# Performance work log

Measured on AMD Instinct MI355X. Metric: run time of the kernel, lower is better.

## Reference

```python
import jax, jax.numpy as jnp
import numpy as np

B, N, C = 4, 2048, 1024
H = 16
D = C // H  # head_dim = 64
SCALE = 1.0 / np.sqrt(D).astype(np.float32)


def setup_inputs() -> dict:
    key = jax.random.key(0)
    ks = jax.random.split(key, 6)
    s = 0.02
    return {
        "x": jax.random.normal(ks[0], (B, N, C), dtype=jnp.float32),
        "Wq": jax.random.normal(ks[1], (C, C), dtype=jnp.float32) * s,
        "Wk": jax.random.normal(ks[2], (C, C), dtype=jnp.float32) * s,
        "Wv": jax.random.normal(ks[3], (C, C), dtype=jnp.float32) * s,
        "Wo": jax.random.normal(ks[4], (C, C), dtype=jnp.float32) * s,
        "bo": jax.random.normal(ks[5], (C,), dtype=jnp.float32) * s,
    }


def reference(x, Wq, Wk, Wv, Wo, bo):
    # q/k/v projections (no bias, qkv_bias=False), split heads -> [B,H,N,D]
    def heads(t):
        return t.reshape(B, N, H, D).transpose(0, 2, 1, 3)
    q = heads(x @ Wq)
    k = heads(x @ Wk)
    v = heads(x @ Wv)
    attn = jnp.einsum("bhnd,bhmd->bhnm", q, k) * SCALE  # [B,H,N,N]
    attn = jax.nn.softmax(attn, axis=-1)
    out = jnp.einsum("bhnm,bhmd->bhnd", attn, v)  # [B,H,N,D]
    out = out.transpose(0, 2, 1, 3).reshape(B, N, C)
    return out @ Wo + bo
```

## Files before the change

kernel.cpp:

```cpp
#include <hip/hip_runtime.h>
#include <hip/hip_bf16.h>


typedef __bf16 bf16x8 __attribute__((ext_vector_type(8)));
typedef __bf16 bf16x4 __attribute__((ext_vector_type(4)));
typedef float  f32x4  __attribute__((ext_vector_type(4)));
typedef float  f32x16 __attribute__((ext_vector_type(16)));
typedef unsigned int u32x4 __attribute__((ext_vector_type(4)));

#define LSCALE 0.18033688f
#define DEFER_THR 8.0f

__device__ __forceinline__ f32x4 mfma16(bf16x8 a, bf16x8 b, f32x4 c) {
    return __builtin_amdgcn_mfma_f32_16x16x32_bf16(a, b, c, 0, 0, 0);
}

__device__ __forceinline__ f32x16 mfma32(bf16x8 a, bf16x8 b, f32x16 c) {
    return __builtin_amdgcn_mfma_f32_32x32x16_bf16(a, b, c, 0, 0, 0);
}

__device__ __forceinline__ unsigned short f2bf(float f) {
    unsigned u = __builtin_bit_cast(unsigned, f);
    u += 0x7fffu + ((u >> 16) & 1u);
    return (unsigned short)(u >> 16);
}

__device__ __forceinline__ unsigned cvt_pk_bf16(float lo, float hi) {
    unsigned r;
    asm("v_cvt_pk_bf16_f32 %0, %1, %2" : "=v"(r) : "v"(lo), "v"(hi));
    return r;
}

__device__ __forceinline__ bf16x4 trread(unsigned addr) {
    bf16x4 d;
    asm volatile("ds_read_b64_tr_b16 %0, %1" : "=v"(d) : "v"(addr));
    return d;
}

__device__ __forceinline__ void gload16(const ushort* g, ushort* l) {
    __builtin_amdgcn_global_load_lds(
        (const __attribute__((address_space(1))) void*)g,
        (__attribute__((address_space(3))) void*)l, 16, 0, 0);
}

__global__ void cast_bf16_kernel(const float4* __restrict__ in,
                                 ushort4* __restrict__ out, int n4) {
    int i = blockIdx.x * blockDim.x + threadIdx.x;
    if (i < n4) {
        float4 f = in[i];
        ushort4 r;
        r.x = f2bf(f.x); r.y = f2bf(f.y); r.z = f2bf(f.z); r.w = f2bf(f.w);
        out[i] = r;
    }
}

__global__ void transpose_cast_kernel(const float* __restrict__ Wq,
                                      const float* __restrict__ Wk,
                                      const float* __restrict__ Wv,
                                      const float* __restrict__ Wo,
                                      ushort* __restrict__ out) {
    __shared__ float tile[32][33];
    const int z = blockIdx.z;
    const float* W = (z == 0) ? Wq : (z == 1) ? Wk : (z == 2) ? Wv : Wo;
    ushort* o = out + (size_t)z * 1024 * 1024;
    const int k0 = blockIdx.x * 32, n0 = blockIdx.y * 32;
    const int tx = threadIdx.x, ty = threadIdx.y;
#pragma unroll
    for (int i = 0; i < 4; i++)
        tile[ty + 8 * i][tx] = W[(size_t)(k0 + ty + 8 * i) * 1024 + n0 + tx];
    __syncthreads();
#pragma unroll
    for (int i = 0; i < 4; i++)
        o[(size_t)(n0 + ty + 8 * i) * 1024 + k0 + tx] = f2bf(tile[tx][ty + 8 * i]);
}

template <int MODE>
__global__ __launch_bounds__(256) void gemm128(const ushort* __restrict__ A,
                                               const ushort* __restrict__ Bt,
                                               ushort* __restrict__ outB,
                                               float* __restrict__ outF,
                                               const float* __restrict__ bias) {
    __shared__ ushort As[128 * 32];
    __shared__ ushort Bs[128 * 32];
    const int tid = threadIdx.x;
    const int lane = tid & 63;
    const int wid = tid >> 6;
    const int wm = wid >> 1, wn = wid & 1;
    const int m0 = blockIdx.x * 128;
    const int n0 = blockIdx.y * 128;
    if (MODE == 0) Bt += (size_t)blockIdx.z * (1024 * 1024);

    f32x4 acc[4][4] = {};

    for (int k0 = 0; k0 < 1024; k0 += 32) {
#pragma unroll
        for (int it = 0; it < 2; ++it) {
            int e = (it * 256 + tid) * 8;
            int r = e >> 5, c = e & 31;
            gload16(&A[(size_t)(m0 + r) * 1024 + k0 + c], &As[e]);
            gload16(&Bt[(size_t)(n0 + r) * 1024 + k0 + c], &Bs[e]);
        }
        __syncthreads();

        bf16x8 a[4], b[4];
#pragma unroll
        for (int i = 0; i < 4; i++) {
            a[i] = *(const bf16x8*)&As[(wm * 64 + i * 16 + (lane & 15)) * 32 + (lane >> 4) * 8];
            b[i] = *(const bf16x8*)&Bs[(wn * 64 + i * 16 + (lane & 15)) * 32 + (lane >> 4) * 8];
        }
#pragma unroll
        for (int i = 0; i < 4; i++)
#pragma unroll
            for (int j = 0; j < 4; j++)
                acc[i][j] = mfma16(a[i], b[j], acc[i][j]);
        __syncthreads();
    }

    const float scl = (MODE == 0 && blockIdx.z == 0) ? LSCALE : 1.0f;
#pragma unroll
    for (int i = 0; i < 4; i++) {
        int row_b = m0 + wm * 64 + i * 16 + ((lane >> 4) * 4);
#pragma unroll
        for (int j = 0; j < 4; j++) {
            int col = n0 + wn * 64 + j * 16 + (lane & 15);
#pragma unroll
            for (int r = 0; r < 4; r++) {
                int row = row_b + r;
                float v = acc[i][j][r] * scl;
                if (MODE == 0) {
                    ushort* o = outB + (size_t)blockIdx.z * (8192ull * 1024);
                    int b = row >> 11, n = row & 2047, h = col >> 6, d = col & 63;
                    o[((((size_t)(b * 16 + h)) * 2048 + n) << 6) + d] = f2bf(v);
                } else {
                    outF[(size_t)row * 1024 + col] = v + bias[col];
                }
            }
        }
    }
}

__global__ __launch_bounds__(256) void attn_kernel(const ushort* __restrict__ Q,
                                                   const ushort* __restrict__ K,
                                                   const ushort* __restrict__ V,
                                                   ushort* __restrict__ O) {
    __shared__ ushort Ks[2][64 * 64];
    __shared__ ushort Vs[2][64 * 64];
    const int tid = threadIdx.x;
    const int lane = tid & 63;
    const int wid = tid >> 6;
    const int hi = lane >> 5;
    const int q32 = lane & 31;
    const int bid = blockIdx.x;
    const int swz = (bid & 7) * 128 + (bid >> 3);
    const int bh = swz >> 4;
    const int qt = swz & 15;
    const size_t base = (size_t)bh * (2048 * 64);

    const int qr = qt * 128 + wid * 32 + q32;
    bf16x8 qf[4];
#pragma unroll
    for (int dc = 0; dc < 4; ++dc)
        qf[dc] = *(const bf16x8*)&Q[base + (size_t)qr * 64 + dc * 16 + hi * 8];

    bf16x8 onesb;
#pragma unroll
    for (int i = 0; i < 8; i++) onesb[i] = (__bf16)1.0f;

    f32x16 o0 = {}, o1 = {}, lacc = {};
    float m_run = -1e30f;

    const int kci0 = tid, kci1 = 256 + tid;
    const int kkey0 = kci0 >> 3, kd0 = (kci0 & 7) * 8;
    const int kkey1 = kci1 >> 3, kd1 = (kci1 & 7) * 8;
    const int kbyt0 = (kkey0 * 128 + kd0 * 2) ^ ((kkey0 & 7) << 4);
    const int kbyt1 = (kkey1 * 128 + kd1 * 2) ^ ((kkey1 & 7) << 4);
    const int vkey0 = (kci0 & 127) >> 1, vd0 = (kci0 >> 7) * 16 + (kci0 & 1) * 8;
    const int vkey1 = (kci1 & 127) >> 1, vd1 = (kci1 >> 7) * 16 + (kci1 & 1) * 8;

    char* const KsB0 = (char*)&Ks[0][0];
    ushort* const Vs0 = &Vs[0][0];
    const unsigned vb0 = (unsigned)(size_t)&Vs[0][0];

    {
        uint4 k0 = *(const uint4*)&K[base + (size_t)kkey0 * 64 + kd0];
        uint4 k1 = *(const uint4*)&K[base + (size_t)kkey1 * 64 + kd1];
        gload16(&V[base + (size_t)vkey0 * 64 + vd0], &Vs0[kci0 * 8]);
        gload16(&V[base + (size_t)vkey1 * 64 + vd1], &Vs0[kci1 * 8]);
        *(uint4*)(KsB0 + kbyt0) = k0;
        *(uint4*)(KsB0 + kbyt1) = k1;
    }
    __syncthreads();

    int cur = 0;
    for (int kt = 0; kt < 2048; kt += 64) {
        const int nxt = cur ^ 1;
        const bool more = (kt + 64) < 2048;
        char* const KsBc = KsB0 + cur * 8192;
        const unsigned vbc = vb0 + cur * 8192;

        uint4 kn0, kn1;
        if (more) {
            const size_t nb = base + (size_t)(kt + 64) * 64;
            gload16(&V[nb + (size_t)vkey0 * 64 + vd0], &Vs0[nxt * 4096 + kci0 * 8]);
            gload16(&V[nb + (size_t)vkey1 * 64 + vd1], &Vs0[nxt * 4096 + kci1 * 8]);
            kn0 = *(const uint4*)&K[nb + (size_t)kkey0 * 64 + kd0];
            kn1 = *(const uint4*)&K[nb + (size_t)kkey1 * 64 + kd1];
        }

        f32x16 s0 = {}, s1 = {};
        __builtin_amdgcn_s_setprio(1);
#pragma unroll
        for (int dc = 0; dc < 4; ++dc) {
            const int dby = (dc * 16 + hi * 8) * 2;
            bf16x8 kf0 = *(const bf16x8*)(KsBc + ((q32 * 128 + dby) ^ ((q32 & 7) << 4)));
            bf16x8 kf1 = *(const bf16x8*)(KsBc + (((32 + q32) * 128 + dby) ^ ((q32 & 7) << 4)));
            s0 = mfma32(kf0, qf[dc], s0);
            s1 = mfma32(kf1, qf[dc], s1);
        }
        __builtin_amdgcn_s_setprio(0);

        float ma = fmaxf(fmaxf(s0[0], s0[1]), fmaxf(s0[2], s0[3]));
        float mb = fmaxf(fmaxf(s0[4], s0[5]), fmaxf(s0[6], s0[7]));
        float mc = fmaxf(fmaxf(s0[8], s0[9]), fmaxf(s0[10], s0[11]));
        float md = fmaxf(fmaxf(s0[12], s0[13]), fmaxf(s0[14], s0[15]));
        float me = fmaxf(fmaxf(s1[0], s1[1]), fmaxf(s1[2], s1[3]));
        float mf = fmaxf(fmaxf(s1[4], s1[5]), fmaxf(s1[6], s1[7]));
        float mg = fmaxf(fmaxf(s1[8], s1[9]), fmaxf(s1[10], s1[11]));
        float mh = fmaxf(fmaxf(s1[12], s1[13]), fmaxf(s1[14], s1[15]));
        float mx = fmaxf(fmaxf(fmaxf(ma, mb), fmaxf(mc, md)),
                         fmaxf(fmaxf(me, mf), fmaxf(mg, mh)));
        mx = fmaxf(mx, __shfl_xor(mx, 32));

        if (!__all(mx <= m_run + DEFER_THR)) {
            float mn2 = fmaxf(m_run, mx);
            float fr = __builtin_amdgcn_exp2f(m_run - mn2);
            m_run = mn2;
#pragma unroll
            for (int r = 0; r < 16; ++r) {
                float f = __shfl(fr, (r & 3) + 8 * (r >> 2) + 4 * hi);
                o0[r] *= f; o1[r] *= f; lacc[r] *= f;
            }
        }
        const float mn = m_run;

#pragma unroll
        for (int t = 0; t < 2; ++t) {
            const f32x16 sv = t ? s1 : s0;

            bf16x4 vv[8];
#pragma unroll
            for (int h2 = 0; h2 < 2; ++h2) {
                const int kb = t * 32 + h2 * 16 + hi * 8;
#pragma unroll
                for (int dt = 0; dt < 2; ++dt) {
                    const int d = dt * 32 + q32;
                    unsigned a = vbc + (d >> 4) * 2048 + kb * 32 + (d & 15) * 8;
                    vv[h2 * 4 + dt * 2 + 0] = trread(a);
                    vv[h2 * 4 + dt * 2 + 1] = trread(a + 128);
                }
            }

            unsigned wA[2][2], wB[2][2];
#pragma unroll
            for (int h2 = 0; h2 < 2; ++h2) {
                float p0 = __builtin_amdgcn_exp2f(sv[8 * h2 + 0] - mn);
                float p1 = __builtin_amdgcn_exp2f(sv[8 * h2 + 1] - mn);
                float p2 = __builtin_amdgcn_exp2f(sv[8 * h2 + 2] - mn);
                float p3 = __builtin_amdgcn_exp2f(sv[8 * h2 + 3] - mn);
                float p4 = __builtin_amdgcn_exp2f(sv[8 * h2 + 4] - mn);
                float p5 = __builtin_amdgcn_exp2f(sv[8 * h2 + 5] - mn);
                float p6 = __builtin_amdgcn_exp2f(sv[8 * h2 + 6] - mn);
                float p7 = __builtin_amdgcn_exp2f(sv[8 * h2 + 7] - mn);
                wA[h2][0] = cvt_pk_bf16(p0, p1);
                wA[h2][1] = cvt_pk_bf16(p2, p3);
                wB[h2][0] = cvt_pk_bf16(p4, p5);
                wB[h2][1] = cvt_pk_bf16(p6, p7);
            }

            asm volatile("s_waitcnt lgkmcnt(0)" ::: "memory");
            __builtin_amdgcn_sched_barrier(0);

            __builtin_amdgcn_s_setprio(1);
#pragma unroll
            for (int h2 = 0; h2 < 2; ++h2) {
                unsigned m0 = hi ? wA[h2][0] : wB[h2][0];
                unsigned m1 = hi ? wA[h2][1] : wB[h2][1];
                unsigned x0 = __shfl_xor(m0, 32);
                unsigned x1 = __shfl_xor(m1, 32);
                u32x4 pw;
                pw.x = hi ? x0 : wA[h2][0];
                pw.y = hi ? x1 : wA[h2][1];
                pw.z = hi ? wB[h2][0] : x0;
                pw.w = hi ? wB[h2][1] : x1;
                bf16x8 pa = __builtin_bit_cast(bf16x8, pw);

                lacc = mfma32(pa, onesb, lacc);
                bf16x8 vf0 = __builtin_shufflevector(vv[h2 * 4 + 0], vv[h2 * 4 + 1],
                                                     0, 1, 2, 3, 4, 5, 6, 7);
                bf16x8 vf1 = __builtin_shufflevector(vv[h2 * 4 + 2], vv[h2 * 4 + 3],
                                                     0, 1, 2, 3, 4, 5, 6, 7);
                o0 = mfma32(pa, vf0, o0);
                o1 = mfma32(pa, vf1, o1);
            }
            __builtin_amdgcn_s_setprio(0);
        }

        if (more) {
            char* const KsBn = KsB0 + nxt * 8192;
            *(uint4*)(KsBn + kbyt0) = kn0;
            *(uint4*)(KsBn + kbyt1) = kn1;
        }
        __syncthreads();
        cur = nxt;
    }

    const int b = bh >> 4, h = bh & 15;
#pragma unroll
    for (int r = 0; r < 16; ++r) {
        float inv = 1.0f / lacc[r];
        int row = qt * 128 + wid * 32 + (r & 3) + 8 * (r >> 2) + 4 * hi;
        size_t rb = (size_t)(b * 2048 + row) * 1024 + h * 64;
        O[rb + q32]      = f2bf(o0[r] * inv);
        O[rb + 32 + q32] = f2bf(o1[r] * inv);
    }
}

extern "C" void kernel_launch(void* const* d_in, const int* in_sizes, int n_in,
                              void* d_out, int out_size, void* d_ws, size_t ws_size,
                              hipStream_t stream) {
    const float* x  = (const float*)d_in[0];
    const float* Wq = (const float*)d_in[1];
    const float* Wk = (const float*)d_in[2];
    const float* Wv = (const float*)d_in[3];
    const float* Wo = (const float*)d_in[4];
    const float* bo = (const float*)d_in[5];
    float* out = (float*)d_out;

    if (ws_size < (size_t)72 * 1024 * 1024) return;
    ushort* ws  = (ushort*)d_ws;
    ushort* xb  = ws;
    ushort* wt  = xb + (size_t)8 * 1024 * 1024;
    ushort* qkv = wt + (size_t)4 * 1024 * 1024;
    ushort* ao  = xb;

    cast_bf16_kernel<<<8192, 256, 0, stream>>>((const float4*)x, (ushort4*)xb,
                                               2 * 1024 * 1024);
    transpose_cast_kernel<<<dim3(32, 32, 4), dim3(32, 8), 0, stream>>>(Wq, Wk, Wv, Wo, wt);
    gemm128<0><<<dim3(64, 8, 3), 256, 0, stream>>>(xb, wt, qkv, nullptr, nullptr);
    attn_kernel<<<1024, 256, 0, stream>>>(
        qkv, qkv + (size_t)8 * 1024 * 1024, qkv + (size_t)16 * 1024 * 1024, ao);
    gemm128<1><<<dim3(64, 8, 1), 256, 0, stream>>>(ao, wt + (size_t)3 * 1024 * 1024,
                                                   nullptr, out, bo);
}
```

Baseline: 218.0 us.

## Replace MFMA row-sum with scalar l accumulation and batch PV MFMAs

Drops the extra MFMA against a ones vector that computed softmax denominators. Each lane now keeps a scalar running sum of its fp32 probabilities and combines the two half-waves at the end. It also hoists all V transposed reads and probability packing for both key halves ahead of a single waitcnt and priority region, and adds a launch-bounds occupancy hint of 4. This removes a third of the PV-phase MFMAs and one synchronisation point, at the cost of more live registers and denominators summed from fp32 rather than bf16-rounded probabilities.

```diff
diff --git a/kernel.cpp b/kernel.cpp
--- a/kernel.cpp
+++ b/kernel.cpp
@@ -139,10 +139,10 @@
     }
 }
 
-__global__ __launch_bounds__(256) void attn_kernel(const ushort* __restrict__ Q,
-                                                   const ushort* __restrict__ K,
-                                                   const ushort* __restrict__ V,
-                                                   ushort* __restrict__ O) {
+__global__ __launch_bounds__(256, 4) void attn_kernel(const ushort* __restrict__ Q,
+                                                      const ushort* __restrict__ K,
+                                                      const ushort* __restrict__ V,
+                                                      ushort* __restrict__ O) {
     __shared__ ushort Ks[2][64 * 64];
     __shared__ ushort Vs[2][64 * 64];
     const int tid = threadIdx.x;
@@ -162,11 +162,8 @@
     for (int dc = 0; dc < 4; ++dc)
         qf[dc] = *(const bf16x8*)&Q[base + (size_t)qr * 64 + dc * 16 + hi * 8];
 
-    bf16x8 onesb;
-#pragma unroll
-    for (int i = 0; i < 8; i++) onesb[i] = (__bf16)1.0f;
-
-    f32x16 o0 = {}, o1 = {}, lacc = {};
+    f32x16 o0 = {}, o1 = {};
+    float l_run = 0.f;
     float m_run = -1e30f;
 
     const int kci0 = tid, kci1 = 256 + tid;
@@ -235,19 +232,18 @@
             float mn2 = fmaxf(m_run, mx);
             float fr = __builtin_amdgcn_exp2f(m_run - mn2);
             m_run = mn2;
+            l_run *= fr;
 #pragma unroll
             for (int r = 0; r < 16; ++r) {
                 float f = __shfl(fr, (r & 3) + 8 * (r >> 2) + 4 * hi);
-                o0[r] *= f; o1[r] *= f; lacc[r] *= f;
+                o0[r] *= f; o1[r] *= f;
             }
         }
         const float mn = m_run;
 
-#pragma unroll
-        for (int t = 0; t < 2; ++t) {
-            const f32x16 sv = t ? s1 : s0;
-
-            bf16x4 vv[8];
+        bf16x4 vv[16];
+#pragma unroll
+        for (int t = 0; t < 2; ++t)
 #pragma unroll
             for (int h2 = 0; h2 < 2; ++h2) {
                 const int kb = t * 32 + h2 * 16 + hi * 8;
@@ -255,12 +251,16 @@
                 for (int dt = 0; dt < 2; ++dt) {
                     const int d = dt * 32 + q32;
                     unsigned a = vbc + (d >> 4) * 2048 + kb * 32 + (d & 15) * 8;
-                    vv[h2 * 4 + dt * 2 + 0] = trread(a);
-                    vv[h2 * 4 + dt * 2 + 1] = trread(a + 128);
+                    vv[t * 8 + h2 * 4 + dt * 2 + 0] = trread(a);
+                    vv[t * 8 + h2 * 4 + dt * 2 + 1] = trread(a + 128);
                 }
             }
 
-            unsigned wA[2][2], wB[2][2];
+        unsigned wA[2][2][2], wB[2][2][2];
+        float tsum = 0.f;
+#pragma unroll
+        for (int t = 0; t < 2; ++t) {
+            const f32x16 sv = t ? s1 : s0;
 #pragma unroll
             for (int h2 = 0; h2 < 2; ++h2) {
                 float p0 = __builtin_amdgcn_exp2f(sv[8 * h2 + 0] - mn);
@@ -271,39 +271,49 @@
                 float p5 = __builtin_amdgcn_exp2f(sv[8 * h2 + 5] - mn);
                 float p6 = __builtin_amdgcn_exp2f(sv[8 * h2 + 6] - mn);
                 float p7 = __builtin_amdgcn_exp2f(sv[8 * h2 + 7] - mn);
-                wA[h2][0] = cvt_pk_bf16(p0, p1);
-                wA[h2][1] = cvt_pk_bf16(p2, p3);
-                wB[h2][0] = cvt_pk_bf16(p4, p5);
-                wB[h2][1] = cvt_pk_bf16(p6, p7);
-            }
-
-            asm volatile("s_waitcnt lgkmcnt(0)" ::: "memory");
-            __builtin_amdgcn_sched_barrier(0);
-
-            __builtin_amdgcn_s_setprio(1);
+                wA[t][h2][0] = cvt_pk_bf16(p0, p1);
+                wA[t][h2][1] = cvt_pk_bf16(p2, p3);
+                wB[t][h2][0] = cvt_pk_bf16(p4, p5);
+                wB[t][h2][1] = cvt_pk_bf16(p6, p7);
+                tsum += ((p0 + p1) + (p2 + p3)) + ((p4 + p5) + (p6 + p7));
+            }
+        }
+        l_run += tsum;
+
+        bf16x8 pa[2][2];
+#pragma unroll
+        for (int t = 0; t < 2; ++t)
 #pragma unroll
             for (int h2 = 0; h2 < 2; ++h2) {
-                unsigned m0 = hi ? wA[h2][0] : wB[h2][0];
-                unsigned m1 = hi ? wA[h2][1] : wB[h2][1];
+                unsigned m0 = hi ? wA[t][h2][0] : wB[t][h2][0];
+                unsigned m1 = hi ? wA[t][h2][1] : wB[t][h2][1];
                 unsigned x0 = __shfl_xor(m0, 32);
                 unsigned x1 = __shfl_xor(m1, 32);
                 u32x4 pw;
-                pw.x = hi ? x0 : wA[h2][0];
-                pw.y = hi ? x1 : wA[h2][1];
-                pw.z = hi ? wB[h2][0] : x0;
-                pw.w = hi ? wB[h2][1] : x1;
-                bf16x8 pa = __builtin_bit_cast(bf16x8, pw);
-
-                lacc = mfma32(pa, onesb, lacc);
-                bf16x8 vf0 = __builtin_shufflevector(vv[h2 * 4 + 0], vv[h2 * 4 + 1],
+                pw.x = hi ? x0 : wA[t][h2][0];
+                pw.y = hi ? x1 : wA[t][h2][1];
+                pw.z = hi ? wB[t][h2][0] : x0;
+                pw.w = hi ? wB[t][h2][1] : x1;
+                pa[t][h2] = __builtin_bit_cast(bf16x8, pw);
+            }
+
+        asm volatile("s_waitcnt lgkmcnt(0)" ::: "memory");
+        __builtin_amdgcn_sched_barrier(0);
+
+        __builtin_amdgcn_s_setprio(1);
+#pragma unroll
+        for (int t = 0; t < 2; ++t)
+#pragma unroll
+            for (int h2 = 0; h2 < 2; ++h2) {
+                const int vbase = t * 8 + h2 * 4;
+                bf16x8 vf0 = __builtin_shufflevector(vv[vbase + 0], vv[vbase + 1],
                                                      0, 1, 2, 3, 4, 5, 6, 7);
-                bf16x8 vf1 = __builtin_shufflevector(vv[h2 * 4 + 2], vv[h2 * 4 + 3],
+                bf16x8 vf1 = __builtin_shufflevector(vv[vbase + 2], vv[vbase + 3],
                                                      0, 1, 2, 3, 4, 5, 6, 7);
-                o0 = mfma32(pa, vf0, o0);
-                o1 = mfma32(pa, vf1, o1);
-            }
-            __builtin_amdgcn_s_setprio(0);
-        }
+                o0 = mfma32(pa[t][h2], vf0, o0);
+                o1 = mfma32(pa[t][h2], vf1, o1);
+            }
+        __builtin_amdgcn_s_setprio(0);
 
         if (more) {
             char* const KsBn = KsB0 + nxt * 8192;
@@ -315,13 +325,16 @@
     }
 
     const int b = bh >> 4, h = bh & 15;
+    float lfull = l_run + __shfl_xor(l_run, 32);
+    float inv = 1.0f / lfull;
 #pragma unroll
     for (int r = 0; r < 16; ++r) {
-        float inv = 1.0f / lacc[r];
-        int row = qt * 128 + wid * 32 + (r & 3) + 8 * (r >> 2) + 4 * hi;
+        int crow = (r & 3) + 8 * (r >> 2) + 4 * hi;
+        float invr = __shfl(inv, crow);
+        int row = qt * 128 + wid * 32 + crow;
         size_t rb = (size_t)(b * 2048 + row) * 1024 + h * 64;
-        O[rb + q32]      = f2bf(o0[r] * inv);
-        O[rb + 32 + q32] = f2bf(o1[r] * inv);
+        O[rb + q32]      = f2bf(o0[r] * invr);
+        O[rb + 32 + q32] = f2bf(o1[r] * invr);
     }
 }
 
```

Measured after the change: 333.8 us. 1.53x slower.
